# Optimization experiments

Measured on AMD Instinct MI355X. Metric: run time of the kernel, lower is better.

The kernel has to match this reference:

```python
import jax, jax.numpy as jnp
import numpy as np
import math

B, L = 2048, 60
D, H, NL = 80, 8, 3
HD = D // H            # head_dim = 10
NLOC, NUSR = 1187, 46
DFF = 2 * D
IN_DIM = D + 24 + 32 + 2   # loc(80)+user(24)+weekday(16)+hour(16)+2 continuous


def _ln(x, g, b):
    m = jnp.mean(x, -1, keepdims=True)
    v = jnp.mean((x - m) ** 2, -1, keepdims=True)
    return (x - m) * jax.lax.rsqrt(v + 1e-5) * g + b


def setup_inputs():
    key = jax.random.key(0)
    k = lambda i: jax.random.fold_in(key, i)
    g = lambda i, shp, s: jax.random.normal(k(i), shp, dtype=jnp.float32) * s
    inp = {
        "loc_seq": jax.random.randint(k(0), (B, L), 0, NLOC),
        "user_seq": jax.random.randint(k(1), (B, L), 0, NUSR),
        "weekday_seq": jax.random.randint(k(2), (B, L), 0, 8),
        "start_min_seq": jax.random.randint(k(3), (B, L), 0, 1440),
        "dur_seq": jax.random.randint(k(4), (B, L), 0, 600),
        "diff_seq": jax.random.randint(k(5), (B, L), 0, 100),
        "seq_len": jax.random.randint(k(6), (B,), 1, L + 1),
    }
    # embedding tables (padding_idx=0 rows zeroed where the module uses it)
    inp["loc_table"] = g(10, (NLOC, D), 0.02).at[0].set(0.0)
    inp["user_table"] = g(11, (NUSR, 24), 0.02).at[0].set(0.0)
    inp["wk_table"] = g(12, (8, 16), 0.02).at[0].set(0.0)
    inp["hr_table"] = g(13, (25, 16), 0.02)
    inp["in_w"] = g(14, (IN_DIM, D), 0.09)
    inp["in_b"] = jnp.zeros((D,), jnp.float32)
    inp["in_g"] = jnp.ones((D,), jnp.float32)
    inp["in_be"] = jnp.zeros((D,), jnp.float32)
    inp["pos_emb"] = g(15, (1, L, D), 0.02)
    # per-layer stacked params (NL=3 layers)
    inp["qkv_w"] = g(16, (NL, D, 3 * D), 0.09)
    inp["proj_w"] = g(17, (NL, D, D), 0.11)
    inp["proj_b"] = jnp.zeros((NL, D), jnp.float32)
    inp["rel_emb"] = g(18, (NL, 2 * L - 1, HD), 1.0)
    inp["n1_g"] = jnp.ones((NL, D), jnp.float32)
    inp["n1_b"] = jnp.zeros((NL, D), jnp.float32)
    inp["ffn_w1"] = g(19, (NL, D, DFF), 0.09)
    inp["ffn_b1"] = jnp.zeros((NL, DFF), jnp.float32)
    inp["ffn_w2"] = g(20, (NL, DFF, D), 0.09)
    inp["ffn_b2"] = jnp.zeros((NL, D), jnp.float32)
    inp["n2_g"] = jnp.ones((NL, D), jnp.float32)
    inp["n2_b"] = jnp.zeros((NL, D), jnp.float32)
    inp["fn_g"] = jnp.ones((D,), jnp.float32)
    inp["fn_b"] = jnp.zeros((D,), jnp.float32)
    inp["pr_w1"] = g(21, (D, D), 0.11)
    inp["pr_b1"] = jnp.zeros((D,), jnp.float32)
    inp["pr_w2"] = g(22, (D, NLOC), 0.04)
    inp["pr_b2"] = jnp.zeros((NLOC,), jnp.float32)
    inp["protos"] = g(23, (NLOC, D), 0.04)
    inp["temp"] = jnp.asarray(2.0, jnp.float32)
    return inp


def reference(loc_seq, user_seq, weekday_seq, start_min_seq, dur_seq, diff_seq, seq_len,
              loc_table, user_table, wk_table, hr_table, in_w, in_b, in_g, in_be, pos_emb,
              qkv_w, proj_w, proj_b, rel_emb, n1_g, n1_b, ffn_w1, ffn_b1, ffn_w2, ffn_b2,
              n2_g, n2_b, fn_g, fn_b, pr_w1, pr_b1, pr_w2, pr_b2, protos, temp):
    Bx, Lx = loc_seq.shape
    loc_e = loc_table[loc_seq]                                            # [B,L,80]
    user_e = jnp.broadcast_to(user_table[user_seq[:, 0]][:, None, :], (Bx, Lx, 24))
    hour = jnp.clip(start_min_seq // 60, 0, 23)
    cont = jnp.stack([diff_seq.astype(jnp.float32) / 10.0,
                      dur_seq.astype(jnp.float32) / 300.0], -1)           # [B,L,2]
    x = jnp.concatenate([loc_e, user_e, wk_table[weekday_seq], hr_table[hour], cont], -1)
    x = _ln(x @ in_w + in_b, in_g, in_be) + pos_emb[:, :Lx, :]
    key_mask = loc_seq == 0                                               # mask keys [B,L]
    pos_idx = jnp.arange(Lx)[None, :] - jnp.arange(Lx)[:, None] + (Lx - 1)  # [L,L]
    scale = 1.0 / math.sqrt(HD)
    for l in range(NL):
        qkv = (x @ qkv_w[l]).reshape(Bx, Lx, 3, H, HD)
        q = qkv[:, :, 0].transpose(0, 2, 1, 3)                            # [B,H,L,hd]
        kk = qkv[:, :, 1].transpose(0, 2, 1, 3)
        v = qkv[:, :, 2].transpose(0, 2, 1, 3)
        rel = rel_emb[l][pos_idx]                                         # [L,L,hd]
        attn = (jnp.einsum('bhid,bhjd->bhij', q, kk)
                + jnp.einsum('bhid,ijd->bhij', q, rel)) * scale
        attn = jnp.where(key_mask[:, None, None, :], -jnp.inf, attn)
        a = jax.nn.softmax(attn, -1)
        o = jnp.einsum('bhij,bhjd->bhid', a, v).transpose(0, 2, 1, 3).reshape(Bx, Lx, D)
        x = _ln(x + o @ proj_w[l] + proj_b[l], n1_g[l], n1_b[l])
        f = jax.nn.gelu(x @ ffn_w1[l] + ffn_b1[l], approximate=False) @ ffn_w2[l] + ffn_b2[l]
        x = _ln(x + f, n2_g[l], n2_b[l])
    x = _ln(x, fn_g, fn_b)
    final = x[jnp.arange(Bx), jnp.clip(seq_len - 1, 0, Lx - 1)]           # [B,80]
    logits_param = jax.nn.gelu(final @ pr_w1 + pr_b1, approximate=False) @ pr_w2 + pr_b2
    fnorm = final / jnp.maximum(jnp.linalg.norm(final, axis=-1, keepdims=True), 1e-12)
    pnorm = protos / jnp.maximum(jnp.linalg.norm(protos, axis=-1, keepdims=True), 1e-12)
    logits = 0.5 * logits_param + 0.5 * (fnorm @ pnorm.T) * 15.0
    return logits / jnp.clip(temp, 0.5, 3.0)
```

## Files before the change

kernel.cpp:

```cpp
#include <hip/hip_runtime.h>
#include <hip/hip_bf16.h>
#include <math.h>

#define BB   2048
#define LL   60
#define DD   80
#define HH   8
#define HDD  10
#define NLNUM 3
#define NLOC 1187
#define DFF  160
#define IN_DIM 138
#define RELN 119
#define SCS  68
#define XP   21
#define HP   41
#define VP   35
#define WSLP 21

__device__ __forceinline__ float gelu_f(float a) {
  float x = fabsf(a) * 0.70710678118654752f;
  float t = 1.0f / (1.0f + 0.3275911f * x);
  float y = t * (0.254829592f + t * (-0.284496736f + t * (1.421413741f +
            t * (-1.453152027f + t * 1.061405429f))));
  float e = 1.0f - y * __expf(-x * x);
  float erf_s = copysignf(e, a);
  return 0.5f * a * (1.0f + erf_s);
}

__global__ __launch_bounds__(256) void k_wprep(
    const float* __restrict__ qkv_w, float* __restrict__ wT) {
  int idx = blockIdx.x * 256 + threadIdx.x;
  if (idx >= 3 * 8 * 30 * 80) return;
  int i = idx % 80;
  int c = (idx / 80) % 30;
  int h = (idx / (80 * 30)) % 8;
  int l = idx / (80 * 30 * 8);
  int col = (c < 10) ? (h * 10 + c)
          : (c < 20) ? (80 + h * 10 + (c - 10))
                     : (160 + h * 10 + (c - 20));
  wT[idx] = qkv_w[(size_t)l * 80 * 240 + (size_t)i * 240 + col];
}

__global__ __launch_bounds__(256) void k_embed(
    const int* __restrict__ loc_seq, const int* __restrict__ user_seq,
    const int* __restrict__ wk_seq, const int* __restrict__ sm_seq,
    const int* __restrict__ dur_seq, const int* __restrict__ diff_seq,
    const float* __restrict__ loc_table, const float* __restrict__ user_table,
    const float* __restrict__ wk_table, const float* __restrict__ hr_table,
    const float* __restrict__ in_w, const float* __restrict__ in_b,
    const float* __restrict__ in_g, const float* __restrict__ in_be,
    const float* __restrict__ pos_emb, float* __restrict__ x) {
  int tok0 = blockIdx.x * 48, tid = threadIdx.x;
  __shared__ __align__(16) float vin[48 * VP * 4];
  __shared__ __align__(16) float ws[140 * 80];
  __shared__ float mstd[96];

  float4* vin4 = (float4*)vin;
  float4* ws4  = (float4*)ws;

  for (int i = tid; i < 140 * 20; i += 256) {
    int r = i / 20, c = i % 20;
    float4 v = make_float4(0.0f, 0.0f, 0.0f, 0.0f);
    if (r < IN_DIM) v = *(const float4*)(in_w + r * 80 + c * 4);
    ws4[i] = v;
  }
  for (int i = tid; i < 48 * 35; i += 256) {
    int t = i / 35, s = i % 35;
    int tok = tok0 + t;
    float4 v;
    if (s < 20) {
      int loc = loc_seq[tok];
      v = *(const float4*)(loc_table + (size_t)loc * 80 + s * 4);
    } else if (s < 26) {
      int usr = user_seq[(tok / LL) * LL];
      v = *(const float4*)(user_table + usr * 24 + (s - 20) * 4);
    } else if (s < 30) {
      int wk = wk_seq[tok];
      v = *(const float4*)(wk_table + wk * 16 + (s - 26) * 4);
    } else if (s < 34) {
      int hr = sm_seq[tok] / 60; hr = min(max(hr, 0), 23);
      v = *(const float4*)(hr_table + hr * 16 + (s - 30) * 4);
    } else {
      v.x = (float)diff_seq[tok] / 10.0f;
      v.y = (float)dur_seq[tok] / 300.0f;
      v.z = 0.0f; v.w = 0.0f;
    }
    vin4[t * VP + s] = v;
  }
  __syncthreads();

  int tg = tid / 20, cg = tid % 20, t0 = tg * 4;
  float acc[4][4] = {};
  if (tid < 240) {
    #pragma unroll 7
    for (int iq = 0; iq < 35; iq++) {
      float4 xv[4], wv[4];
      #pragma unroll
      for (int dt = 0; dt < 4; dt++) xv[dt] = vin4[(t0 + dt) * VP + iq];
      #pragma unroll
      for (int di = 0; di < 4; di++) wv[di] = ws4[(iq * 4 + di) * 20 + cg];
      #pragma unroll
      for (int dt = 0; dt < 4; dt++) {
        const float* xp = (const float*)&xv[dt];
        #pragma unroll
        for (int di = 0; di < 4; di++) {
          const float* wp = (const float*)&wv[di];
          #pragma unroll
          for (int dc = 0; dc < 4; dc++) acc[dt][dc] += xp[di] * wp[dc];
        }
      }
    }
  }
  __syncthreads();
  if (tid < 240) {
    float4 bb = *(const float4*)(in_b + cg * 4);
    const float* bp = (const float*)&bb;
    #pragma unroll
    for (int dt = 0; dt < 4; dt++) {
      float4 y;
      y.x = acc[dt][0] + bp[0];
      y.y = acc[dt][1] + bp[1];
      y.z = acc[dt][2] + bp[2];
      y.w = acc[dt][3] + bp[3];
      vin4[(t0 + dt) * VP + cg] = y;
    }
  }
  __syncthreads();
  if (tid < 48) {
    float s = 0.0f, s2 = 0.0f;
    #pragma unroll
    for (int iq = 0; iq < 20; iq++) {
      float4 v = vin4[tid * VP + iq];
      s  += v.x + v.y + v.z + v.w;
      s2 += v.x * v.x + v.y * v.y + v.z * v.z + v.w * v.w;
    }
    float mean = s / 80.0f;
    float var  = fmaxf(s2 / 80.0f - mean * mean, 0.0f);
    mstd[tid] = mean; mstd[48 + tid] = rsqrtf(var + 1e-5f);
  }
  __syncthreads();
  for (int e = tid; e < 960; e += 256) {
    int t = e / 20, c4 = e % 20;
    float4 v = vin4[t * VP + c4];
    float4 gg = *(const float4*)(in_g + c4 * 4);
    float4 bb = *(const float4*)(in_be + c4 * 4);
    float4 pe = *(const float4*)(pos_emb + ((tok0 + t) % LL) * 80 + c4 * 4);
    float m = mstd[t], r = mstd[48 + t];
    float4 out;
    out.x = (v.x - m) * r * gg.x + bb.x + pe.x;
    out.y = (v.y - m) * r * gg.y + bb.y + pe.y;
    out.z = (v.z - m) * r * gg.z + bb.z + pe.z;
    out.w = (v.w - m) * r * gg.w + bb.w + pe.w;
    ((float4*)(x + (size_t)tok0 * 80))[e] = out;
  }
}

__global__ __launch_bounds__(256) void k_battn(
    const float* __restrict__ x, const int* __restrict__ loc_seq,
    const float* __restrict__ wT,
    const float* __restrict__ rel_emb,
    float* __restrict__ o) {
  int b = blockIdx.x, tid = threadIdx.x;

  __shared__ __align__(16) float xs[LL * XP * 4];
  __shared__ __align__(16) float qkvh[30 * 60];
  __shared__ __align__(16) float scbuf[LL * SCS];
  __shared__ __align__(16) float relT[HDD * 120];
  __shared__ __align__(16) float rsum[64];
  __shared__ float msk[60];

  float4* xs4  = (float4*)xs;
  float4* wsl4 = (float4*)scbuf;
  float* sc    = scbuf;

  const float4* xb4 = (const float4*)(x + (size_t)b * 4800);
  for (int i = tid; i < 1200; i += 256) xs4[(i / 20) * XP + (i % 20)] = xb4[i];
  for (int i = tid; i < RELN * HDD; i += 256) {
    int d = i / RELN, p = i % RELN;
    relT[d * 120 + p] = rel_emb[p * 10 + d];
  }
  if (tid < 60) msk[tid] = (loc_seq[b * LL + tid] == 0) ? 1.0f : 0.0f;

  for (int h = 0; h < HH; h++) {
    __syncthreads();
    const float4* w4 = (const float4*)(wT + (size_t)h * 2400);
    for (int i = tid; i < 600; i += 256)
      wsl4[(i / 20) * WSLP + (i % 20)] = w4[i];
    __syncthreads();

    if (tid < 225) {
      int ct = tid / 15, tt = tid % 15;
      int c2 = ct * 2, t0 = tt * 4;
      float acc[2][4] = {};
      #pragma unroll 5
      for (int iq = 0; iq < 20; iq++) {
        float4 wv0 = wsl4[c2 * WSLP + iq];
        float4 wv1 = wsl4[(c2 + 1) * WSLP + iq];
        const float* w0 = (const float*)&wv0;
        const float* w1 = (const float*)&wv1;
        #pragma unroll
        for (int dt = 0; dt < 4; dt++) {
          float4 xv = xs4[(t0 + dt) * XP + iq];
          const float* xp = (const float*)&xv;
          #pragma unroll
          for (int di = 0; di < 4; di++) {
            acc[0][dt] += w0[di] * xp[di];
            acc[1][dt] += w1[di] * xp[di];
          }
        }
      }
      *(float4*)(qkvh + c2 * 60 + t0) =
          make_float4(acc[0][0], acc[0][1], acc[0][2], acc[0][3]);
      *(float4*)(qkvh + (c2 + 1) * 60 + t0) =
          make_float4(acc[1][0], acc[1][1], acc[1][2], acc[1][3]);
    }
    __syncthreads();

    const float* qs = qkvh;
    const float* ks = qkvh + 600;
    if (tid < 225) {
      int ig = tid / 15, jg = tid % 15;
      int i0 = ig * 4, j0 = jg * 4;
      int w0 = j0 - i0 + 56;
      float acc[4][4] = {};
      #pragma unroll
      for (int d = 0; d < 10; d++) {
        float4 qv = *(const float4*)(qs + d * 60 + i0);
        float4 kv = *(const float4*)(ks + d * 60 + j0);
        float4 rA = *(const float4*)(relT + d * 120 + w0);
        float4 rB = *(const float4*)(relT + d * 120 + w0 + 4);
        float rr[8] = {rA.x, rA.y, rA.z, rA.w, rB.x, rB.y, rB.z, rB.w};
        const float* qp = (const float*)&qv;
        const float* kp = (const float*)&kv;
        #pragma unroll
        for (int di = 0; di < 4; di++)
          #pragma unroll
          for (int dj = 0; dj < 4; dj++)
            acc[di][dj] += qp[di] * (kp[dj] + rr[dj - di + 3]);
      }
      const float scale = 0.31622776601683794f;
      #pragma unroll
      for (int di = 0; di < 4; di++) {
        #pragma unroll
        for (int dj = 0; dj < 4; dj++) {
          float v = acc[di][dj] * scale;
          if (msk[j0 + dj] != 0.0f) v = -1e30f;
          acc[di][dj] = v;
        }
        *(float4*)(sc + (i0 + di) * SCS + j0) =
            make_float4(acc[di][0], acc[di][1], acc[di][2], acc[di][3]);
      }
    }
    __syncthreads();

    if (tid < 240) {
      int r = tid >> 2, q = tid & 3;
      float* row = sc + r * SCS;
      float4 vbuf[4];
      float m = -3.0e38f;
      #pragma unroll
      for (int s = 0; s < 4; s++) {
        int k = q + 4 * s;
        if (k < 15) {
          float4 v = *(const float4*)(row + 4 * k);
          vbuf[s] = v;
          m = fmaxf(m, fmaxf(fmaxf(v.x, v.y), fmaxf(v.z, v.w)));
        }
      }
      m = fmaxf(m, __shfl_xor(m, 1));
      m = fmaxf(m, __shfl_xor(m, 2));
      float sum = 0.0f;
      #pragma unroll
      for (int s = 0; s < 4; s++) {
        int k = q + 4 * s;
        if (k < 15) {
          float4 v = vbuf[s];
          v.x = __expf(v.x - m); v.y = __expf(v.y - m);
          v.z = __expf(v.z - m); v.w = __expf(v.w - m);
          *(float4*)(row + 4 * k) = v;
          sum += v.x + v.y + v.z + v.w;
        }
      }
      sum += __shfl_xor(sum, 1);
      sum += __shfl_xor(sum, 2);
      if (q == 0) rsum[r] = 1.0f / sum;
    }
    __syncthreads();

    if (tid < 150) {
      int ig = tid / 10, d = tid % 10;
      const float* vsr = qkvh + 1200 + d * 60;
      float acc[4] = {0, 0, 0, 0};
      #pragma unroll 5
      for (int jq = 0; jq < 15; jq++) {
        float4 vv = *(const float4*)(vsr + jq * 4);
        #pragma unroll
        for (int di = 0; di < 4; di++) {
          float4 av = *(const float4*)(sc + (ig + 15 * di) * SCS + jq * 4);
          acc[di] += av.x * vv.x + av.y * vv.y + av.z * vv.z + av.w * vv.w;
        }
      }
      #pragma unroll
      for (int di = 0; di < 4; di++) {
        int t = ig + 15 * di;
        o[((size_t)b * 60 + t) * 80 + h * 10 + d] = acc[di] * rsum[t];
      }
    }
  }
}

__global__ __launch_bounds__(256) void k_proj_ln(
    const float* __restrict__ o, const float* __restrict__ proj_w,
    const float* __restrict__ proj_b, const float* __restrict__ g,
    const float* __restrict__ be, float* __restrict__ x) {
  int tok0 = blockIdx.x * 48, tid = threadIdx.x;
  __shared__ __align__(16) float os[48 * XP * 4];
  __shared__ __align__(16) float ws[80 * 80];
  __shared__ float mstd[96];

  float4* os4 = (float4*)os;
  const float4* ob4 = (const float4*)(o + (size_t)tok0 * 80);
  for (int i = tid; i < 960; i += 256) os4[(i / 20) * XP + (i % 20)] = ob4[i];
  float4* ws4 = (float4*)ws;
  for (int i = tid; i < 1600; i += 256)
    ws4[i] = *(const float4*)(proj_w + (i / 20) * 80 + (i % 20) * 4);
  __syncthreads();

  int tg = tid / 20, cg = tid % 20, t0 = tg * 4;
  float acc[4][4] = {};
  if (tid < 240) {
    #pragma unroll
    for (int iq = 0; iq < 20; iq++) {
      float4 xv[4], wv[4];
      #pragma unroll
      for (int dt = 0; dt < 4; dt++) xv[dt] = os4[(t0 + dt) * XP + iq];
      #pragma unroll
      for (int di = 0; di < 4; di++) wv[di] = ws4[(iq * 4 + di) * 20 + cg];
      #pragma unroll
      for (int dt = 0; dt < 4; dt++) {
        const float* xp = (const float*)&xv[dt];
        #pragma unroll
        for (int di = 0; di < 4; di++) {
          const float* wp = (const float*)&wv[di];
          #pragma unroll
          for (int dc = 0; dc < 4; dc++) acc[dt][dc] += xp[di] * wp[dc];
        }
      }
    }
  }
  __syncthreads();
  if (tid < 240) {
    float4 pb = *(const float4*)(proj_b + cg * 4);
    const float* pbp = (const float*)&pb;
    #pragma unroll
    for (int dt = 0; dt < 4; dt++) {
      float4 xr = *(const float4*)(x + (size_t)(tok0 + t0 + dt) * 80 + cg * 4);
      const float* xrp = (const float*)&xr;
      float4 out;
      out.x = acc[dt][0] + pbp[0] + xrp[0];
      out.y = acc[dt][1] + pbp[1] + xrp[1];
      out.z = acc[dt][2] + pbp[2] + xrp[2];
      out.w = acc[dt][3] + pbp[3] + xrp[3];
      os4[(t0 + dt) * XP + cg] = out;
    }
  }
  __syncthreads();
  if (tid < 48) {
    float s = 0.0f, s2 = 0.0f;
    #pragma unroll
    for (int iq = 0; iq < 20; iq++) {
      float4 v = os4[tid * XP + iq];
      s  += v.x + v.y + v.z + v.w;
      s2 += v.x * v.x + v.y * v.y + v.z * v.z + v.w * v.w;
    }
    float mean = s / 80.0f;
    float var  = fmaxf(s2 / 80.0f - mean * mean, 0.0f);
    mstd[tid] = mean; mstd[48 + tid] = rsqrtf(var + 1e-5f);
  }
  __syncthreads();
  for (int e = tid; e < 960; e += 256) {
    int t = e / 20, c4 = e % 20;
    float4 v = os4[t * XP + c4];
    float4 gg = *(const float4*)(g + c4 * 4);
    float4 bb = *(const float4*)(be + c4 * 4);
    float m = mstd[t], r = mstd[48 + t];
    float4 out;
    out.x = (v.x - m) * r * gg.x + bb.x;
    out.y = (v.y - m) * r * gg.y + bb.y;
    out.z = (v.z - m) * r * gg.z + bb.z;
    out.w = (v.w - m) * r * gg.w + bb.w;
    ((float4*)(x + (size_t)tok0 * 80))[e] = out;
  }
}

__global__ __launch_bounds__(256) void k_ffn(
    const float* __restrict__ w1, const float* __restrict__ b1,
    const float* __restrict__ w2, const float* __restrict__ b2,
    const float* __restrict__ g, const float* __restrict__ be,
    float* __restrict__ x) {
  int tok0 = blockIdx.x * 48, tid = threadIdx.x;
  __shared__ __align__(16) float xs[48 * XP * 4];
  __shared__ __align__(16) float hs[48 * HP * 4];
  __shared__ __align__(16) float ws[80 * 80];
  __shared__ float mstd[96];

  float4* xs4 = (float4*)xs;
  float4* hs4 = (float4*)hs;
  float4* ws4 = (float4*)ws;
  const float4* xb4 = (const float4*)(x + (size_t)tok0 * 80);
  for (int i = tid; i < 960; i += 256) xs4[(i / 20) * XP + (i % 20)] = xb4[i];

  int tg = tid / 20, cg = tid % 20, t0 = tg * 4;

  for (int c0 = 0; c0 < 160; c0 += 80) {
    __syncthreads();
    for (int i = tid; i < 1600; i += 256)
      ws4[i] = *(const float4*)(w1 + (i / 20) * 160 + c0 + (i % 20) * 4);
    __syncthreads();
    if (tid < 240) {
      float acc[4][4] = {};
      #pragma unroll
      for (int iq = 0; iq < 20; iq++) {
        float4 xv[4], wv[4];
        #pragma unroll
        for (int dt = 0; dt < 4; dt++) xv[dt] = xs4[(t0 + dt) * XP + iq];
        #pragma unroll
        for (int di = 0; di < 4; di++) wv[di] = ws4[(iq * 4 + di) * 20 + cg];
        #pragma unroll
        for (int dt = 0; dt < 4; dt++) {
          const float* xp = (const float*)&xv[dt];
          #pragma unroll
          for (int di = 0; di < 4; di++) {
            const float* wp = (const float*)&wv[di];
            #pragma unroll
            for (int dc = 0; dc < 4; dc++) acc[dt][dc] += xp[di] * wp[dc];
          }
        }
      }
      float4 bb = *(const float4*)(b1 + c0 + cg * 4);
      const float* bp = (const float*)&bb;
      #pragma unroll
      for (int dt = 0; dt < 4; dt++) {
        float4 out;
        float* op = (float*)&out;
        #pragma unroll
        for (int dc = 0; dc < 4; dc++)
          op[dc] = gelu_f(acc[dt][dc] + bp[dc]);
        hs4[(t0 + dt) * HP + c0 / 4 + cg] = out;
      }
    }
  }

  float acc[4][4] = {};
  for (int k0 = 0; k0 < 160; k0 += 80) {
    __syncthreads();
    for (int i = tid; i < 1600; i += 256)
      ws4[i] = *(const float4*)(w2 + (size_t)(k0 + i / 20) * 80 + (i % 20) * 4);
    __syncthreads();
    if (tid < 240) {
      #pragma unroll
      for (int iq = 0; iq < 20; iq++) {
        float4 hv[4], wv[4];
        #pragma unroll
        for (int dt = 0; dt < 4; dt++) hv[dt] = hs4[(t0 + dt) * HP + k0 / 4 + iq];
        #pragma unroll
        for (int di = 0; di < 4; di++) wv[di] = ws4[(iq * 4 + di) * 20 + cg];
        #pragma unroll
        for (int dt = 0; dt < 4; dt++) {
          const float* hp = (const float*)&hv[dt];
          #pragma unroll
          for (int di = 0; di < 4; di++) {
            const float* wp = (const float*)&wv[di];
            #pragma unroll
            for (int dc = 0; dc < 4; dc++) acc[dt][dc] += hp[di] * wp[dc];
          }
        }
      }
    }
  }
  __syncthreads();
  if (tid < 240) {
    float4 bb = *(const float4*)(b2 + cg * 4);
    const float* bp = (const float*)&bb;
    #pragma unroll
    for (int dt = 0; dt < 4; dt++) {
      float4 xr = xs4[(t0 + dt) * XP + cg];
      const float* xrp = (const float*)&xr;
      float4 out;
      out.x = acc[dt][0] + bp[0] + xrp[0];
      out.y = acc[dt][1] + bp[1] + xrp[1];
      out.z = acc[dt][2] + bp[2] + xrp[2];
      out.w = acc[dt][3] + bp[3] + xrp[3];
      hs4[(t0 + dt) * HP + cg] = out;
    }
  }
  __syncthreads();
  if (tid < 48) {
    float s = 0.0f, s2 = 0.0f;
    #pragma unroll
    for (int iq = 0; iq < 20; iq++) {
      float4 v = hs4[tid * HP + iq];
      s  += v.x + v.y + v.z + v.w;
      s2 += v.x * v.x + v.y * v.y + v.z * v.z + v.w * v.w;
    }
    float mean = s / 80.0f;
    float var  = fmaxf(s2 / 80.0f - mean * mean, 0.0f);
    mstd[tid] = mean; mstd[48 + tid] = rsqrtf(var + 1e-5f);
  }
  __syncthreads();
  for (int e = tid; e < 960; e += 256) {
    int t = e / 20, c4 = e % 20;
    float4 v = hs4[t * HP + c4];
    float4 gg = *(const float4*)(g + c4 * 4);
    float4 bb = *(const float4*)(be + c4 * 4);
    float m = mstd[t], r = mstd[48 + t];
    float4 out;
    out.x = (v.x - m) * r * gg.x + bb.x;
    out.y = (v.y - m) * r * gg.y + bb.y;
    out.z = (v.z - m) * r * gg.z + bb.z;
    out.w = (v.w - m) * r * gg.w + bb.w;
    ((float4*)(x + (size_t)tok0 * 80))[e] = out;
  }
}

__global__ __launch_bounds__(128) void k_final(
    const float* __restrict__ x, const int* __restrict__ seq_len,
    const float* __restrict__ fn_g, const float* __restrict__ fn_b,
    const float* __restrict__ pr_w1, const float* __restrict__ pr_b1,
    float* __restrict__ fnorm, float* __restrict__ h1) {
  int b = blockIdx.x, tid = threadIdx.x;
  __shared__ float red[128], red2[128];
  __shared__ float fbuf[DD];
  int t = seq_len[b] - 1; t = min(max(t, 0), LL - 1);
  float v = 0.0f;
  if (tid < DD) v = x[((size_t)b * LL + t) * DD + tid];
  red[tid]  = (tid < DD) ? v : 0.0f;
  red2[tid] = (tid < DD) ? v * v : 0.0f;
  __syncthreads();
  for (int s = 64; s > 0; s >>= 1) {
    if (tid < s) { red[tid] += red[tid + s]; red2[tid] += red2[tid + s]; }
    __syncthreads();
  }
  float mean = red[0] / DD;
  float var  = fmaxf(red2[0] / DD - mean * mean, 0.0f);
  float rstd = rsqrtf(var + 1e-5f);
  float f = 0.0f;
  if (tid < DD) { f = (v - mean) * rstd * fn_g[tid] + fn_b[tid]; fbuf[tid] = f; }
  __syncthreads();
  red[tid] = (tid < DD) ? f * f : 0.0f;
  __syncthreads();
  for (int s = 64; s > 0; s >>= 1) {
    if (tid < s) red[tid] += red[tid + s];
    __syncthreads();
  }
  float rn = 1.0f / fmaxf(sqrtf(red[0]), 1e-12f);
  if (tid < DD) {
    fnorm[(size_t)b * DD + tid] = f * rn;
    float gacc = pr_b1[tid];
    for (int i = 0; i < DD; i++) gacc += fbuf[i] * pr_w1[i * DD + tid];
    h1[(size_t)b * DD + tid] = gelu_f(gacc);
  }
}

__global__ __launch_bounds__(128) void k_pnorm(
    const float* __restrict__ protos, float* __restrict__ pnormT) {
  int c = blockIdx.x, tid = threadIdx.x;
  __shared__ float red[128];
  float v = 0.0f;
  if (tid < DD) v = protos[(size_t)c * DD + tid];
  red[tid] = (tid < DD) ? v * v : 0.0f;
  __syncthreads();
  for (int s = 64; s > 0; s >>= 1) {
    if (tid < s) red[tid] += red[tid + s];
    __syncthreads();
  }
  float rn = 1.0f / fmaxf(sqrtf(red[0]), 1e-12f);
  if (tid < DD) pnormT[(size_t)tid * NLOC + c] = v * rn;
}

__global__ __launch_bounds__(256) void k_logits(
    const float* __restrict__ h1, const float* __restrict__ fnorm,
    const float* __restrict__ pr_w2, const float* __restrict__ pr_b2,
    const float* __restrict__ pnormT, const float* __restrict__ temp,
    float* __restrict__ out) {
  int b = blockIdx.x / 5, cb = blockIdx.x % 5;
  int tid = threadIdx.x;
  int c = cb * 256 + tid;
  __shared__ float h1s[DD], fns[DD];
  if (tid < DD) { h1s[tid] = h1[(size_t)b * DD + tid]; fns[tid] = fnorm[(size_t)b * DD + tid]; }
  __syncthreads();
  if (c < NLOC) {
    float a1 = pr_b2[c], a2 = 0.0f;
    for (int k = 0; k < DD; k++) {
      a1 += h1s[k] * pr_w2[(size_t)k * NLOC + c];
      a2 += fns[k] * pnormT[(size_t)k * NLOC + c];
    }
    float tt = fminf(fmaxf(temp[0], 0.5f), 3.0f);
    out[(size_t)b * NLOC + c] = (0.5f * a1 + 7.5f * a2) / tt;
  }
}

extern "C" void kernel_launch(void* const* d_in, const int* in_sizes, int n_in,
                              void* d_out, int out_size, void* d_ws, size_t ws_size,
                              hipStream_t stream) {
  const int* loc_seq   = (const int*)d_in[0];
  const int* user_seq  = (const int*)d_in[1];
  const int* wk_seq    = (const int*)d_in[2];
  const int* sm_seq    = (const int*)d_in[3];
  const int* dur_seq   = (const int*)d_in[4];
  const int* diff_seq  = (const int*)d_in[5];
  const int* seq_len   = (const int*)d_in[6];
  const float* loc_table = (const float*)d_in[7];
  const float* user_table= (const float*)d_in[8];
  const float* wk_table  = (const float*)d_in[9];
  const float* hr_table  = (const float*)d_in[10];
  const float* in_w   = (const float*)d_in[11];
  const float* in_b   = (const float*)d_in[12];
  const float* in_g   = (const float*)d_in[13];
  const float* in_be  = (const float*)d_in[14];
  const float* pos_emb= (const float*)d_in[15];
  const float* qkv_w  = (const float*)d_in[16];
  const float* proj_w = (const float*)d_in[17];
  const float* proj_b = (const float*)d_in[18];
  const float* rel_emb= (const float*)d_in[19];
  const float* n1_g   = (const float*)d_in[20];
  const float* n1_b   = (const float*)d_in[21];
  const float* ffn_w1 = (const float*)d_in[22];
  const float* ffn_b1 = (const float*)d_in[23];
  const float* ffn_w2 = (const float*)d_in[24];
  const float* ffn_b2 = (const float*)d_in[25];
  const float* n2_g   = (const float*)d_in[26];
  const float* n2_b   = (const float*)d_in[27];
  const float* fn_g   = (const float*)d_in[28];
  const float* fn_b   = (const float*)d_in[29];
  const float* pr_w1  = (const float*)d_in[30];
  const float* pr_b1  = (const float*)d_in[31];
  const float* pr_w2  = (const float*)d_in[32];
  const float* pr_b2  = (const float*)d_in[33];
  const float* protos = (const float*)d_in[34];
  const float* temp   = (const float*)d_in[35];
  float* out = (float*)d_out;

  float* x      = (float*)d_ws;
  float* o      = x + (size_t)BB * LL * DD;
  float* wT     = o + (size_t)BB * LL * DD;
  float* fnorm  = wT + 57600;
  float* h1     = fnorm + (size_t)BB * DD;
  float* pnormT = h1 + (size_t)BB * DD;

  k_wprep<<<225, 256, 0, stream>>>(qkv_w, wT);

  k_embed<<<BB * LL / 48, 256, 0, stream>>>(loc_seq, user_seq, wk_seq, sm_seq,
                                            dur_seq, diff_seq, loc_table,
                                            user_table, wk_table, hr_table,
                                            in_w, in_b, in_g, in_be, pos_emb, x);

  for (int l = 0; l < NLNUM; l++) {
    k_battn<<<BB, 256, 0, stream>>>(x, loc_seq, wT + (size_t)l * 8 * 30 * 80,
                                    rel_emb + (size_t)l * RELN * HDD, o);
    k_proj_ln<<<BB * LL / 48, 256, 0, stream>>>(o, proj_w + (size_t)l * DD * DD,
                                                proj_b + (size_t)l * DD,
                                                n1_g + (size_t)l * DD,
                                                n1_b + (size_t)l * DD, x);
    k_ffn<<<BB * LL / 48, 256, 0, stream>>>(ffn_w1 + (size_t)l * DD * DFF,
                                            ffn_b1 + (size_t)l * DFF,
                                            ffn_w2 + (size_t)l * DFF * DD,
                                            ffn_b2 + (size_t)l * DD,
                                            n2_g + (size_t)l * DD,
                                            n2_b + (size_t)l * DD, x);
  }

  k_pnorm<<<NLOC, 128, 0, stream>>>(protos, pnormT);
  k_final<<<BB, 128, 0, stream>>>(x, seq_len, fn_g, fn_b, pr_w1, pr_b1, fnorm, h1);
  k_logits<<<BB * 5, 256, 0, stream>>>(h1, fnorm, pr_w2, pr_b2, pnormT, temp, out);
}
```

Baseline: 1.703 ms.

## Re-tile per-head attention: padded weight layout, 4x4 QKV tiles, transposed scores

The QKV weights are re-laid out as [l][h][i][32 columns], padded with zeros, so each thread can compute a 4-column by 4-token tile with float4 weight loads. That uses 120 threads instead of 225 with 2x4 tiles. Scores are now stored transposed, so the softmax runs one thread per query row over a strided column, and the AV product reads contiguous float4s across queries. This is meant to raise register reuse and cut LDS traffic, at the cost of less parallelism in the QKV and softmax phases.

```diff
diff --git a/kernel.cpp b/kernel.cpp
--- a/kernel.cpp
+++ b/kernel.cpp
@@ -16,7 +16,6 @@
 #define XP   21
 #define HP   41
 #define VP   35
-#define WSLP 21
 
 __device__ __forceinline__ float gelu_f(float a) {
   float x = fabsf(a) * 0.70710678118654752f;
@@ -31,15 +30,19 @@
 __global__ __launch_bounds__(256) void k_wprep(
     const float* __restrict__ qkv_w, float* __restrict__ wT) {
   int idx = blockIdx.x * 256 + threadIdx.x;
-  if (idx >= 3 * 8 * 30 * 80) return;
-  int i = idx % 80;
-  int c = (idx / 80) % 30;
-  int h = (idx / (80 * 30)) % 8;
-  int l = idx / (80 * 30 * 8);
-  int col = (c < 10) ? (h * 10 + c)
-          : (c < 20) ? (80 + h * 10 + (c - 10))
-                     : (160 + h * 10 + (c - 20));
-  wT[idx] = qkv_w[(size_t)l * 80 * 240 + (size_t)i * 240 + col];
+  if (idx >= 61440) return;
+  int c = idx & 31;
+  int i = (idx >> 5) % 80;
+  int h = ((idx >> 5) / 80) % 8;
+  int l = idx / (32 * 80 * 8);
+  float v = 0.0f;
+  if (c < 30) {
+    int col = (c < 10) ? (h * 10 + c)
+            : (c < 20) ? (80 + h * 10 + (c - 10))
+                       : (160 + h * 10 + (c - 20));
+    v = qkv_w[(size_t)l * 19200 + (size_t)i * 240 + col];
+  }
+  wT[idx] = v;
 }
 
 __global__ __launch_bounds__(256) void k_embed(
@@ -164,15 +167,15 @@
   int b = blockIdx.x, tid = threadIdx.x;
 
   __shared__ __align__(16) float xs[LL * XP * 4];
-  __shared__ __align__(16) float qkvh[30 * 60];
+  __shared__ __align__(16) float qkvh[32 * 60];
   __shared__ __align__(16) float scbuf[LL * SCS];
   __shared__ __align__(16) float relT[HDD * 120];
   __shared__ __align__(16) float rsum[64];
   __shared__ float msk[60];
 
   float4* xs4  = (float4*)xs;
-  float4* wsl4 = (float4*)scbuf;
-  float* sc    = scbuf;
+  float4* wst4 = (float4*)scbuf;
+  float* scT   = scbuf;
 
   const float4* xb4 = (const float4*)(x + (size_t)b * 4800);
   for (int i = tid; i < 1200; i += 256) xs4[(i / 20) * XP + (i % 20)] = xb4[i];
@@ -184,50 +187,49 @@
 
   for (int h = 0; h < HH; h++) {
     __syncthreads();
-    const float4* w4 = (const float4*)(wT + (size_t)h * 2400);
-    for (int i = tid; i < 600; i += 256)
-      wsl4[(i / 20) * WSLP + (i % 20)] = w4[i];
-    __syncthreads();
-
-    if (tid < 225) {
-      int ct = tid / 15, tt = tid % 15;
-      int c2 = ct * 2, t0 = tt * 4;
-      float acc[2][4] = {};
+    const float4* w4 = (const float4*)(wT + (size_t)h * 2560);
+    for (int i = tid; i < 640; i += 256) wst4[i] = w4[i];
+    __syncthreads();
+
+    if (tid < 120) {
+      int cg = tid & 7, tg = tid >> 3;
+      int c0 = cg * 4, t0 = tg * 4;
+      float acc[4][4] = {};
       #pragma unroll 5
       for (int iq = 0; iq < 20; iq++) {
-        float4 wv0 = wsl4[c2 * WSLP + iq];
-        float4 wv1 = wsl4[(c2 + 1) * WSLP + iq];
-        const float* w0 = (const float*)&wv0;
-        const float* w1 = (const float*)&wv1;
-        #pragma unroll
-        for (int dt = 0; dt < 4; dt++) {
-          float4 xv = xs4[(t0 + dt) * XP + iq];
-          const float* xp = (const float*)&xv;
+        float4 xv[4], wv[4];
+        #pragma unroll
+        for (int dt = 0; dt < 4; dt++) xv[dt] = xs4[(t0 + dt) * XP + iq];
+        #pragma unroll
+        for (int di = 0; di < 4; di++) wv[di] = wst4[(iq * 4 + di) * 8 + cg];
+        #pragma unroll
+        for (int di = 0; di < 4; di++) {
+          const float* wp = (const float*)&wv[di];
           #pragma unroll
-          for (int di = 0; di < 4; di++) {
-            acc[0][dt] += w0[di] * xp[di];
-            acc[1][dt] += w1[di] * xp[di];
+          for (int dt = 0; dt < 4; dt++) {
+            const float* xp = (const float*)&xv[dt];
+            #pragma unroll
+            for (int dc = 0; dc < 4; dc++)
+              acc[dc][dt] += wp[dc] * xp[di];
           }
         }
       }
-      *(float4*)(qkvh + c2 * 60 + t0) =
-          make_float4(acc[0][0], acc[0][1], acc[0][2], acc[0][3]);
-      *(float4*)(qkvh + (c2 + 1) * 60 + t0) =
-          make_float4(acc[1][0], acc[1][1], acc[1][2], acc[1][3]);
-    }
-    __syncthreads();
-
-    const float* qs = qkvh;
-    const float* ks = qkvh + 600;
+      #pragma unroll
+      for (int dc = 0; dc < 4; dc++)
+        *(float4*)(qkvh + (c0 + dc) * 60 + t0) =
+            make_float4(acc[dc][0], acc[dc][1], acc[dc][2], acc[dc][3]);
+    }
+    __syncthreads();
+
     if (tid < 225) {
-      int ig = tid / 15, jg = tid % 15;
+      int ig = tid % 15, jg = tid / 15;
       int i0 = ig * 4, j0 = jg * 4;
       int w0 = j0 - i0 + 56;
       float acc[4][4] = {};
       #pragma unroll
       for (int d = 0; d < 10; d++) {
-        float4 qv = *(const float4*)(qs + d * 60 + i0);
-        float4 kv = *(const float4*)(ks + d * 60 + j0);
+        float4 qv = *(const float4*)(qkvh + d * 60 + i0);
+        float4 kv = *(const float4*)(qkvh + 600 + d * 60 + j0);
         float4 rA = *(const float4*)(relT + d * 120 + w0);
         float4 rB = *(const float4*)(relT + d * 120 + w0 + 4);
         float rr[8] = {rA.x, rA.y, rA.z, rA.w, rB.x, rB.y, rB.z, rB.w};
@@ -241,69 +243,53 @@
       }
       const float scale = 0.31622776601683794f;
       #pragma unroll
-      for (int di = 0; di < 4; di++) {
-        #pragma unroll
-        for (int dj = 0; dj < 4; dj++) {
-          float v = acc[di][dj] * scale;
-          if (msk[j0 + dj] != 0.0f) v = -1e30f;
-          acc[di][dj] = v;
-        }
-        *(float4*)(sc + (i0 + di) * SCS + j0) =
-            make_float4(acc[di][0], acc[di][1], acc[di][2], acc[di][3]);
-      }
-    }
-    __syncthreads();
-
-    if (tid < 240) {
-      int r = tid >> 2, q = tid & 3;
-      float* row = sc + r * SCS;
-      float4 vbuf[4];
+      for (int dj = 0; dj < 4; dj++) {
+        float mk = msk[j0 + dj];
+        float4 col;
+        col.x = (mk != 0.0f) ? -1e30f : acc[0][dj] * scale;
+        col.y = (mk != 0.0f) ? -1e30f : acc[1][dj] * scale;
+        col.z = (mk != 0.0f) ? -1e30f : acc[2][dj] * scale;
+        col.w = (mk != 0.0f) ? -1e30f : acc[3][dj] * scale;
+        *(float4*)(scT + (j0 + dj) * SCS + i0) = col;
+      }
+    }
+    __syncthreads();
+
+    if (tid < 60) {
       float m = -3.0e38f;
-      #pragma unroll
-      for (int s = 0; s < 4; s++) {
-        int k = q + 4 * s;
-        if (k < 15) {
-          float4 v = *(const float4*)(row + 4 * k);
-          vbuf[s] = v;
-          m = fmaxf(m, fmaxf(fmaxf(v.x, v.y), fmaxf(v.z, v.w)));
-        }
-      }
-      m = fmaxf(m, __shfl_xor(m, 1));
-      m = fmaxf(m, __shfl_xor(m, 2));
+      #pragma unroll 10
+      for (int j = 0; j < 60; j++) m = fmaxf(m, scT[j * SCS + tid]);
       float sum = 0.0f;
-      #pragma unroll
-      for (int s = 0; s < 4; s++) {
-        int k = q + 4 * s;
-        if (k < 15) {
-          float4 v = vbuf[s];
-          v.x = __expf(v.x - m); v.y = __expf(v.y - m);
-          v.z = __expf(v.z - m); v.w = __expf(v.w - m);
-          *(float4*)(row + 4 * k) = v;
-          sum += v.x + v.y + v.z + v.w;
-        }
-      }
-      sum += __shfl_xor(sum, 1);
-      sum += __shfl_xor(sum, 2);
-      if (q == 0) rsum[r] = 1.0f / sum;
+      #pragma unroll 10
+      for (int j = 0; j < 60; j++) {
+        float e = __expf(scT[j * SCS + tid] - m);
+        scT[j * SCS + tid] = e;
+        sum += e;
+      }
+      rsum[tid] = 1.0f / sum;
     }
     __syncthreads();
 
     if (tid < 150) {
-      int ig = tid / 10, d = tid % 10;
+      int ig = tid % 15, d = tid / 15;
+      int i0 = 4 * ig;
       const float* vsr = qkvh + 1200 + d * 60;
       float acc[4] = {0, 0, 0, 0};
       #pragma unroll 5
       for (int jq = 0; jq < 15; jq++) {
         float4 vv = *(const float4*)(vsr + jq * 4);
-        #pragma unroll
-        for (int di = 0; di < 4; di++) {
-          float4 av = *(const float4*)(sc + (ig + 15 * di) * SCS + jq * 4);
-          acc[di] += av.x * vv.x + av.y * vv.y + av.z * vv.z + av.w * vv.w;
+        const float* vp = (const float*)&vv;
+        #pragma unroll
+        for (int dj = 0; dj < 4; dj++) {
+          float4 scv = *(const float4*)(scT + (4 * jq + dj) * SCS + i0);
+          const float* sp = (const float*)&scv;
+          #pragma unroll
+          for (int di = 0; di < 4; di++) acc[di] += sp[di] * vp[dj];
         }
       }
       #pragma unroll
       for (int di = 0; di < 4; di++) {
-        int t = ig + 15 * di;
+        int t = i0 + di;
         o[((size_t)b * 60 + t) * 80 + h * 10 + d] = acc[di] * rsum[t];
       }
     }
@@ -645,11 +631,11 @@
   float* x      = (float*)d_ws;
   float* o      = x + (size_t)BB * LL * DD;
   float* wT     = o + (size_t)BB * LL * DD;
-  float* fnorm  = wT + 57600;
+  float* fnorm  = wT + 61440;
   float* h1     = fnorm + (size_t)BB * DD;
   float* pnormT = h1 + (size_t)BB * DD;
 
-  k_wprep<<<225, 256, 0, stream>>>(qkv_w, wT);
+  k_wprep<<<240, 256, 0, stream>>>(qkv_w, wT);
 
   k_embed<<<BB * LL / 48, 256, 0, stream>>>(loc_seq, user_seq, wk_seq, sm_seq,
                                             dur_seq, diff_seq, loc_table,
@@ -657,7 +643,7 @@
                                             in_w, in_b, in_g, in_be, pos_emb, x);
 
   for (int l = 0; l < NLNUM; l++) {
-    k_battn<<<BB, 256, 0, stream>>>(x, loc_seq, wT + (size_t)l * 8 * 30 * 80,
+    k_battn<<<BB, 256, 0, stream>>>(x, loc_seq, wT + (size_t)l * 20480,
                                     rel_emb + (size_t)l * RELN * HDD, o);
     k_proj_ln<<<BB * LL / 48, 256, 0, stream>>>(o, proj_w + (size_t)l * DD * DD,
                                                 proj_b + (size_t)l * DD,
```

New measurement: 2.011 ms. 1.18x slower.
